# Optimization experiments

Measured on AMD Instinct MI355X. Metric: run time of the kernel, lower is better.

Reference implementation:

```python
import jax, jax.numpy as jnp
import numpy as np

E, I, H, T = 8, 2816, 1024, 8192

def setup_inputs() -> dict:
    key = jax.random.key(0)
    ks = jax.random.split(key, 5)
    scale_w = 1.0 / np.sqrt(H)
    return {
        "hidden_states": jax.random.normal(ks[0], (T, H), jnp.float32),
        "router_logits": jax.random.normal(ks[1], (T, E), jnp.float32),
        "W1": jax.random.normal(ks[2], (E, I, H), jnp.float32) * scale_w,
        "W3": jax.random.normal(ks[3], (E, I, H), jnp.float32) * scale_w,
        "W2": jax.random.normal(ks[4], (E, H, I), jnp.float32) * (1.0 / np.sqrt(I)),
        "top_k": 2,
    }

def reference(hidden_states, router_logits, W1, W3, W2, top_k):
    # softmax router in fp32, topk, renormalize (renormalize=True, use_grouped_topk=False)
    probs = jax.nn.softmax(router_logits.astype(jnp.float32), axis=-1)  # [T,E]
    vals, idx = jax.lax.top_k(probs, top_k)                             # [T,K]
    vals = vals / jnp.sum(vals, axis=-1, keepdims=True)
    vals = vals.astype(hidden_states.dtype)
    n_tok, n_exp = probs.shape
    # dense per-token expert weight matrix [T,E]; zero for unrouted experts,
    # mathematically identical to the gather/scatter-add in the ipex op
    w = jnp.zeros((n_tok, n_exp), hidden_states.dtype).at[
        jnp.arange(n_tok)[:, None], idx].add(vals)

    def expert_step(acc, args):
        We1, We3, We2, we = args  # [I,H], [I,H], [H,I], [T]
        h = jax.nn.silu(hidden_states @ We1.T) * (hidden_states @ We3.T)  # [T,I]
        return acc + we[:, None] * (h @ We2.T), None

    out, _ = jax.lax.scan(expert_step, jnp.zeros_like(hidden_states),
                          (W1, W3, W2, w.T))
    return out
```

## Files before the change

### kernel.cpp

```cpp
#include <hip/hip_runtime.h>
#include <stdint.h>

#define NE 8
#define NI 2816
#define NH 1024
#define NT 8192
#define NPAIR (NT * 2)

typedef __bf16 bf16x8 __attribute__((ext_vector_type(8)));
typedef float f32x4 __attribute__((ext_vector_type(4)));

__device__ __forceinline__ uint16_t f2bf(float f) {
    union { float f; uint32_t u; } v;
    v.f = f;
    return (uint16_t)((v.u + 0x7FFFu + ((v.u >> 16) & 1u)) >> 16);
}

__device__ __forceinline__ float bflo(uint32_t u) {
    union { uint32_t x; float f; } v; v.x = u << 16; return v.f;
}
__device__ __forceinline__ float bfhi(uint32_t u) {
    union { uint32_t x; float f; } v; v.x = u & 0xffff0000u; return v.f;
}

__device__ __forceinline__ void gld16(const void* g, void* l) {
    __builtin_amdgcn_global_load_lds(
        (__attribute__((address_space(1))) void*)(uintptr_t)g,
        (__attribute__((address_space(3))) void*)(uint32_t)(uintptr_t)l,
        16, 0, 0);
}

__global__ __launch_bounds__(256) void k_cvt_w13(const float* __restrict__ W1,
                                                 const float* __restrict__ W3,
                                                 uint16_t* __restrict__ Wg) {
    int row = blockIdx.x * 2 + (threadIdx.x >> 7);
    int g = threadIdx.x & 127;
    const float* src = (blockIdx.y == 0) ? W1 : W3;
    int e = row / NI;
    int r = row - e * NI;
    size_t drow = (size_t)e * (2 * NI) + (size_t)((r >> 4) * 32 + (r & 15) + (blockIdx.y ? 16 : 0));
    const float4* sp = (const float4*)(src + (size_t)row * NH);
    float4 a = sp[g * 2];
    float4 b = sp[g * 2 + 1];
    uint4 o;
    o.x = (uint32_t)f2bf(a.x) | ((uint32_t)f2bf(a.y) << 16);
    o.y = (uint32_t)f2bf(a.z) | ((uint32_t)f2bf(a.w) << 16);
    o.z = (uint32_t)f2bf(b.x) | ((uint32_t)f2bf(b.y) << 16);
    o.w = (uint32_t)f2bf(b.z) | ((uint32_t)f2bf(b.w) << 16);
    ((uint4*)(Wg + drow * NH))[g] = o;
}

__global__ __launch_bounds__(256) void k_cvt_flat(const float* __restrict__ S,
                                                  uint16_t* __restrict__ D) {
    size_t i = (size_t)blockIdx.x * 256 + threadIdx.x;
    float4 a = ((const float4*)S)[i * 2];
    float4 b = ((const float4*)S)[i * 2 + 1];
    uint4 o;
    o.x = (uint32_t)f2bf(a.x) | ((uint32_t)f2bf(a.y) << 16);
    o.y = (uint32_t)f2bf(a.z) | ((uint32_t)f2bf(a.w) << 16);
    o.z = (uint32_t)f2bf(b.x) | ((uint32_t)f2bf(b.y) << 16);
    o.w = (uint32_t)f2bf(b.z) | ((uint32_t)f2bf(b.w) << 16);
    ((uint4*)D)[i] = o;
}

__global__ __launch_bounds__(256) void k_router(const float* __restrict__ logits,
                                                int* __restrict__ tok_e,
                                                float2* __restrict__ tok_w,
                                                int* __restrict__ counts) {
    int t = blockIdx.x * 256 + threadIdx.x;
    if (t >= NT) return;
    float4 a = ((const float4*)logits)[(size_t)t * 2];
    float4 b = ((const float4*)logits)[(size_t)t * 2 + 1];
    float l[8] = {a.x, a.y, a.z, a.w, b.x, b.y, b.z, b.w};
    int i0 = 0; float l0 = l[0];
#pragma unroll
    for (int e = 1; e < 8; e++) if (l[e] > l0) { l0 = l[e]; i0 = e; }
    int i1 = -1; float l1 = -3.4e38f;
#pragma unroll
    for (int e = 0; e < 8; e++) if (e != i0 && l[e] > l1) { l1 = l[e]; i1 = e; }
    float w0 = 1.f / (1.f + __expf(l1 - l0));
    float w1 = 1.f - w0;
    tok_e[t] = i0 | (i1 << 8);
    tok_w[t] = make_float2(w0, w1);
    atomicAdd(&counts[i0], 1);
    atomicAdd(&counts[i1], 1);
}

__global__ void k_scan(const int* __restrict__ counts, int* __restrict__ offsets,
                       int* __restrict__ cursor) {
    if (threadIdx.x == 0) {
        int o = 0;
        for (int e = 0; e < NE; e++) { offsets[e] = o; cursor[e] = o; o += counts[e]; }
    }
}

__global__ __launch_bounds__(128) void k_gather(const float* __restrict__ x,
                                                const int* __restrict__ tok_e,
                                                const float2* __restrict__ tok_w,
                                                int* __restrict__ cursor,
                                                uint16_t* __restrict__ Xg,
                                                int2* __restrict__ tok_slots,
                                                float* __restrict__ slot_w) {
    int t = blockIdx.x;
    __shared__ int ss[2];
    if (threadIdx.x == 0) {
        int ee = tok_e[t];
        float2 w = tok_w[t];
        int s0 = atomicAdd(&cursor[ee & 0xff], 1);
        int s1 = atomicAdd(&cursor[(ee >> 8) & 0xff], 1);
        ss[0] = s0; ss[1] = s1;
        tok_slots[t] = make_int2(s0, s1);
        slot_w[s0] = w.x;
        slot_w[s1] = w.y;
    }
    __syncthreads();
    int s0 = ss[0], s1 = ss[1];
    int i = threadIdx.x;
    const float4* xr = (const float4*)(x + (size_t)t * NH);
    float4 a = xr[i * 2];
    float4 b = xr[i * 2 + 1];
    uint4 o;
    o.x = (uint32_t)f2bf(a.x) | ((uint32_t)f2bf(a.y) << 16);
    o.y = (uint32_t)f2bf(a.z) | ((uint32_t)f2bf(a.w) << 16);
    o.z = (uint32_t)f2bf(b.x) | ((uint32_t)f2bf(b.y) << 16);
    o.w = (uint32_t)f2bf(b.z) | ((uint32_t)f2bf(b.w) << 16);
    ((uint4*)(Xg + (size_t)s0 * NH))[i] = o;
    ((uint4*)(Xg + (size_t)s1 * NH))[i] = o;
}


#define BAR()  asm volatile("s_barrier" ::: "memory")
#define WAITLGKM asm volatile("s_waitcnt lgkmcnt(0)" ::: "memory")
#define WAITV4 asm volatile("s_waitcnt vmcnt(4)" ::: "memory")
#define WAITV0 asm volatile("s_waitcnt vmcnt(0)" ::: "memory")
#define SCHB __builtin_amdgcn_sched_barrier(0)
#define PRIO1 __builtin_amdgcn_s_setprio(1)
#define PRIO0 __builtin_amdgcn_s_setprio(0)

#define STAGE(ab, bufsel, h, kt)                                                  \
    do {                                                                          \
        char* d_ = lds + (bufsel) * 65536 + (ab) * 32768 + (h) * 16384 + tid * 16; \
        gld16(((ab) ? srcB : srcA)[h][0] + (kt) * 64, d_);                         \
        gld16(((ab) ? srcB : srcA)[h][1] + (kt) * 64, d_ + 8192);                  \
    } while (0)

#define READA(bufsel, mh)                                                           \
    do {                                                                            \
        _Pragma("unroll") for (int ii = 0; ii < 4; ii++) {                          \
            const char* p_ = lds + (bufsel) * 65536 + wr * 16384 +                  \
                             (((mh) * 4 + ii) * 16 + l15) * 128;                    \
            af[ii][0] = *(const bf16x8*)(p_ + colk0);                               \
            af[ii][1] = *(const bf16x8*)(p_ + colk1);                               \
        }                                                                           \
    } while (0)

#define READB(bufsel, nh, dst)                                                      \
    do {                                                                            \
        _Pragma("unroll") for (int jj = 0; jj < 2; jj++) {                          \
            int gb_ = wc * 64 + ((nh) * 2 + jj) * 16;                               \
            const char* p_ = lds + (bufsel) * 65536 + 32768 + (gb_ >> 7) * 16384 +  \
                             ((gb_ & 127) + l15) * 128;                             \
            dst[jj][0] = *(const bf16x8*)(p_ + colk0);                              \
            dst[jj][1] = *(const bf16x8*)(p_ + colk1);                              \
        }                                                                           \
    } while (0)

#define MMQ(mh, bsrc, jb)                                                           \
    do {                                                                            \
        _Pragma("unroll") for (int ii = 0; ii < 4; ii++)                            \
            _Pragma("unroll") for (int jj = 0; jj < 2; jj++)                        \
                _Pragma("unroll") for (int ks = 0; ks < 2; ks++)                    \
                    acc[(mh) * 4 + ii][(jb) + jj] =                                 \
                        __builtin_amdgcn_mfma_f32_16x16x32_bf16(                    \
                            af[ii][ks], bsrc[jj][ks], acc[(mh) * 4 + ii][(jb) + jj],\
                            0, 0, 0);                                               \
    } while (0)

#define PHASES(i2, LAST)                                                            \
    do {                                                                            \
        int t1_ = (i2) + 1, t2_ = (i2) + 2, t3_ = (i2) + 3;                         \
                                                                            \
        READA(0, 0); READB(0, 0, b0);                                               \
        STAGE(0, 1, 0, t1_); STAGE(0, 1, 1, t1_);                                   \
        BAR(); WAITLGKM; SCHB; PRIO1; MMQ(0, b0, 0); PRIO0; SCHB; BAR();            \
                                                                            \
        READB(0, 1, b1);                                                            \
        BAR(); WAITLGKM; SCHB; PRIO1; MMQ(0, b1, 2); PRIO0; SCHB; BAR();            \
                                                                            \
        READA(0, 1);                                                                \
        if (!(LAST)) STAGE(1, 0, 0, t2_);                                           \
        BAR(); WAITLGKM; SCHB; PRIO1; MMQ(1, b1, 2); PRIO0; SCHB; BAR();            \
                                                                            \
        if (!(LAST)) STAGE(1, 0, 1, t2_);                                           \
        BAR(); PRIO1; MMQ(1, b0, 0); PRIO0; SCHB;                                   \
        if (LAST) { WAITV0; } else { WAITV4; }                                      \
        BAR();                                                                      \
                                                                            \
        READA(1, 0); READB(1, 0, b0);                                               \
        if (!(LAST)) { STAGE(0, 0, 0, t2_); STAGE(0, 0, 1, t2_); }                  \
        BAR(); WAITLGKM; SCHB; PRIO1; MMQ(0, b0, 0); PRIO0; SCHB; BAR();            \
                                                                            \
        READB(1, 1, b1);                                                            \
        BAR(); WAITLGKM; SCHB; PRIO1; MMQ(0, b1, 2); PRIO0; SCHB; BAR();            \
                                                                            \
        READA(1, 1);                                                                \
        if (!(LAST)) STAGE(1, 1, 0, t3_);                                           \
        BAR(); WAITLGKM; SCHB; PRIO1; MMQ(1, b1, 2); PRIO0; SCHB; BAR();            \
                                                                            \
        if (!(LAST)) STAGE(1, 1, 1, t3_);                                           \
        BAR(); PRIO1; MMQ(1, b0, 0); PRIO0; SCHB;                                   \
        if (LAST) { WAITV0; } else { WAITV4; }                                      \
        BAR();                                                                      \
    } while (0)

template <int MODE>
__global__ __launch_bounds__(512, 2) void k_moe_gemm(const uint16_t* __restrict__ Abase,
                                                     const uint16_t* __restrict__ Bbase,
                                                     uint16_t* __restrict__ Cbase,
                                                     const int* __restrict__ counts,
                                                     const int* __restrict__ offsets) {
    constexpr int K = (MODE == 1) ? NH : NI;
    constexpr int NKT = K / 64;
    constexpr int NITER = NKT / 2;
    constexpr int BROWS = (MODE == 1) ? 2 * NI : NH;
    constexpr int CLD = (MODE == 1) ? NI : NH;

    int e = blockIdx.z;
    int n_e = counts[e];
    int mtile = blockIdx.y;
    if (mtile * 256 >= n_e) return;
    int ntile = blockIdx.x;
    int off = offsets[e];

    __shared__ __align__(16) char lds[131072];

    int tid = threadIdx.x;
    int l15 = tid & 15;
    int q = (tid >> 4) & 3;
    int x7 = tid & 7;
    int wv = tid >> 6, wr = wv >> 2, wc = wv & 3;
    int colk0 = (q ^ x7) << 4;
    int colk1 = ((q + 4) ^ x7) << 4;

    int sr = tid >> 3;
    int ss = x7 ^ (sr & 7);
    const uint16_t* srcA[2][2];
    const uint16_t* srcB[2][2];
#pragma unroll
    for (int h = 0; h < 2; h++)
#pragma unroll
        for (int j = 0; j < 2; j++) {
            int gr = off + mtile * 256 + h * 128 + j * 64 + sr;
            gr = min(gr, NPAIR - 1);
            srcA[h][j] = Abase + (size_t)gr * K + ss * 8;
            int gn = ntile * 256 + h * 128 + j * 64 + sr;
            srcB[h][j] = Bbase + (size_t)e * BROWS * K + (size_t)gn * K + ss * 8;
        }

    bf16x8 af[4][2], b0[2][2], b1[2][2];
    f32x4 acc[8][4] = {};

    STAGE(0, 0, 0, 0); STAGE(0, 0, 1, 0);
    STAGE(1, 0, 0, 0); STAGE(1, 0, 1, 0);
    STAGE(1, 1, 0, 1); STAGE(1, 1, 1, 1);
    WAITV4;
    BAR();

#pragma unroll 1
    for (int it2 = 0; it2 < NITER - 1; it2++) { PHASES(2 * it2, 0); }
    PHASES(2 * (NITER - 1), 1);

    int sBase = off + mtile * 256;
    if constexpr (MODE == 1) {
#pragma unroll
        for (int im = 0; im < 8; im++) {
#pragma unroll
            for (int r = 0; r < 4; r++) {
                int lm = wr * 128 + im * 16 + q * 4 + r;
                if (mtile * 256 + lm < n_e) {
                    uint16_t* orow = Cbase + (size_t)(sBase + lm) * CLD +
                                     ntile * 128 + wc * 32 + l15;
#pragma unroll
                    for (int j = 0; j < 2; j++) {
                        float c1 = acc[im][2 * j][r];
                        float c3 = acc[im][2 * j + 1][r];
                        float hv = (c1 / (1.f + __expf(-c1))) * c3;
                        orow[j * 16] = f2bf(hv);
                    }
                }
            }
        }
    } else {
#pragma unroll
        for (int im = 0; im < 8; im++) {
#pragma unroll
            for (int r = 0; r < 4; r++) {
                int lm = wr * 128 + im * 16 + q * 4 + r;
                if (mtile * 256 + lm < n_e) {
                    uint16_t* orow = Cbase + (size_t)(sBase + lm) * CLD +
                                     ntile * 256 + wc * 64 + l15;
#pragma unroll
                    for (int jn = 0; jn < 4; jn++) orow[jn * 16] = f2bf(acc[im][jn][r]);
                }
            }
        }
    }
}

__global__ __launch_bounds__(256) void k_combine(const uint16_t* __restrict__ Y,
                                                 const int2* __restrict__ tok_slots,
                                                 const float* __restrict__ slot_w,
                                                 float* __restrict__ out) {
    int idx = blockIdx.x * 256 + threadIdx.x;
    int t = idx >> 7;
    int g = idx & 127;
    int2 s = tok_slots[t];
    float w0 = slot_w[s.x], w1 = slot_w[s.y];
    uint4 u0 = ((const uint4*)(Y + (size_t)s.x * NH))[g];
    uint4 u1 = ((const uint4*)(Y + (size_t)s.y * NH))[g];
    float4 o0, o1;
    o0.x = w0 * bflo(u0.x) + w1 * bflo(u1.x);
    o0.y = w0 * bfhi(u0.x) + w1 * bfhi(u1.x);
    o0.z = w0 * bflo(u0.y) + w1 * bflo(u1.y);
    o0.w = w0 * bfhi(u0.y) + w1 * bfhi(u1.y);
    o1.x = w0 * bflo(u0.z) + w1 * bflo(u1.z);
    o1.y = w0 * bfhi(u0.z) + w1 * bfhi(u1.z);
    o1.z = w0 * bflo(u0.w) + w1 * bflo(u1.w);
    o1.w = w0 * bfhi(u0.w) + w1 * bfhi(u1.w);
    float4* orow = (float4*)(out + (size_t)t * NH + g * 8);
    orow[0] = o0;
    orow[1] = o1;
}

extern "C" void kernel_launch(void* const* d_in, const int* in_sizes, int n_in,
                              void* d_out, int out_size, void* d_ws, size_t ws_size,
                              hipStream_t stream) {
    const float* x = (const float*)d_in[0];
    const float* logits = (const float*)d_in[1];
    const float* W1 = (const float*)d_in[2];
    const float* W3 = (const float*)d_in[3];
    const float* W2 = (const float*)d_in[4];
    float* out = (float*)d_out;

    char* ws = (char*)d_ws;
    size_t o = 0;
    auto nxt = [&](size_t b) -> void* {
        void* p = ws + o;
        o += (b + 255) & ~(size_t)255;
        return p;
    };
    const size_t WELEMS = (size_t)NE * NI * NH;
    uint16_t* Wg = (uint16_t*)nxt(WELEMS * 2 * 2);
    uint16_t* W2b = (uint16_t*)nxt(WELEMS * 2);
    uint16_t* Xg = (uint16_t*)nxt((size_t)NPAIR * NH * 2);
    uint16_t* Hbuf = (uint16_t*)nxt((size_t)NPAIR * NI * 2);
    float* slot_w = (float*)nxt((size_t)NPAIR * 4);
    int2* tok_slots = (int2*)nxt((size_t)NT * 8);
    int* tok_e = (int*)nxt((size_t)NT * 4);
    float2* tok_w = (float2*)nxt((size_t)NT * 8);
    int* meta = (int*)nxt(128);
    int* counts = meta;
    int* offsets = meta + 8;
    int* cursor = meta + 16;
    uint16_t* Ybuf = Xg;
    (void)ws_size; (void)in_sizes; (void)n_in;

    hipMemsetAsync(meta, 0, 128, stream);

    k_router<<<NT / 256, 256, 0, stream>>>(logits, tok_e, tok_w, counts);
    k_scan<<<1, 64, 0, stream>>>(counts, offsets, cursor);

    k_cvt_w13<<<dim3(NE * NI / 2, 2), 256, 0, stream>>>(W1, W3, Wg);
    k_cvt_flat<<<(unsigned)(WELEMS / 8 / 256), 256, 0, stream>>>(W2, W2b);

    k_gather<<<NT, 128, 0, stream>>>(x, tok_e, tok_w, cursor, Xg, tok_slots, slot_w);

    k_moe_gemm<1><<<dim3(2 * NI / 256, NT / 256, NE), 512, 0, stream>>>(
        Xg, Wg, Hbuf, counts, offsets);
    k_moe_gemm<2><<<dim3(NH / 256, NT / 256, NE), 512, 0, stream>>>(
        Hbuf, W2b, Ybuf, counts, offsets);

    k_combine<<<NT * NH / 8 / 256, 256, 0, stream>>>(Ybuf, tok_slots, slot_w, out);
}
```

Baseline: 907.2 us.

## Restructure GEMM main loop into deeper staggered LDS prefetch pipeline

Replaces the two-phase PHASES macro with a single loop that issues one quarter-tile global-to-LDS stage per MFMA sub-phase and keeps more loads in flight (vmcnt 6 instead of 4). LDS reads for both B halves are issued up front and waited on partially (lgkmcnt 4), and the number of barriers per iteration drops from two per sub-phase to one. The goal is to overlap global loads and LDS reads more closely with MFMA work and cut barrier stalls. The trailing iterations clamp k-tile indices, so they issue redundant loads instead of branching, which risks extra traffic and subtle hazards from buffer reuse.

```diff
diff --git a/kernel.cpp b/kernel.cpp
--- a/kernel.cpp
+++ b/kernel.cpp
@@ -130,8 +130,9 @@
 
 
 #define BAR()  asm volatile("s_barrier" ::: "memory")
-#define WAITLGKM asm volatile("s_waitcnt lgkmcnt(0)" ::: "memory")
-#define WAITV4 asm volatile("s_waitcnt vmcnt(4)" ::: "memory")
+#define WAITLGKM0 asm volatile("s_waitcnt lgkmcnt(0)" ::: "memory")
+#define WAITLGKM4 asm volatile("s_waitcnt lgkmcnt(4)" ::: "memory")
+#define WAITV6 asm volatile("s_waitcnt vmcnt(6)" ::: "memory")
 #define WAITV0 asm volatile("s_waitcnt vmcnt(0)" ::: "memory")
 #define SCHB __builtin_amdgcn_sched_barrier(0)
 #define PRIO1 __builtin_amdgcn_s_setprio(1)
@@ -174,43 +175,6 @@
                         __builtin_amdgcn_mfma_f32_16x16x32_bf16(                    \
                             af[ii][ks], bsrc[jj][ks], acc[(mh) * 4 + ii][(jb) + jj],\
                             0, 0, 0);                                               \
-    } while (0)
-
-#define PHASES(i2, LAST)                                                            \
-    do {                                                                            \
-        int t1_ = (i2) + 1, t2_ = (i2) + 2, t3_ = (i2) + 3;                         \
-                                                                            \
-        READA(0, 0); READB(0, 0, b0);                                               \
-        STAGE(0, 1, 0, t1_); STAGE(0, 1, 1, t1_);                                   \
-        BAR(); WAITLGKM; SCHB; PRIO1; MMQ(0, b0, 0); PRIO0; SCHB; BAR();            \
-                                                                            \
-        READB(0, 1, b1);                                                            \
-        BAR(); WAITLGKM; SCHB; PRIO1; MMQ(0, b1, 2); PRIO0; SCHB; BAR();            \
-                                                                            \
-        READA(0, 1);                                                                \
-        if (!(LAST)) STAGE(1, 0, 0, t2_);                                           \
-        BAR(); WAITLGKM; SCHB; PRIO1; MMQ(1, b1, 2); PRIO0; SCHB; BAR();            \
-                                                                            \
-        if (!(LAST)) STAGE(1, 0, 1, t2_);                                           \
-        BAR(); PRIO1; MMQ(1, b0, 0); PRIO0; SCHB;                                   \
-        if (LAST) { WAITV0; } else { WAITV4; }                                      \
-        BAR();                                                                      \
-                                                                            \
-        READA(1, 0); READB(1, 0, b0);                                               \
-        if (!(LAST)) { STAGE(0, 0, 0, t2_); STAGE(0, 0, 1, t2_); }                  \
-        BAR(); WAITLGKM; SCHB; PRIO1; MMQ(0, b0, 0); PRIO0; SCHB; BAR();            \
-                                                                            \
-        READB(1, 1, b1);                                                            \
-        BAR(); WAITLGKM; SCHB; PRIO1; MMQ(0, b1, 2); PRIO0; SCHB; BAR();            \
-                                                                            \
-        READA(1, 1);                                                                \
-        if (!(LAST)) STAGE(1, 1, 0, t3_);                                           \
-        BAR(); WAITLGKM; SCHB; PRIO1; MMQ(1, b1, 2); PRIO0; SCHB; BAR();            \
-                                                                            \
-        if (!(LAST)) STAGE(1, 1, 1, t3_);                                           \
-        BAR(); PRIO1; MMQ(1, b0, 0); PRIO0; SCHB;                                   \
-        if (LAST) { WAITV0; } else { WAITV4; }                                      \
-        BAR();                                                                      \
     } while (0)
 
 template <int MODE>
@@ -260,15 +224,58 @@
     bf16x8 af[4][2], b0[2][2], b1[2][2];
     f32x4 acc[8][4] = {};
 
-    STAGE(0, 0, 0, 0); STAGE(0, 0, 1, 0);
-    STAGE(1, 0, 0, 0); STAGE(1, 0, 1, 0);
-    STAGE(1, 1, 0, 1); STAGE(1, 1, 1, 1);
-    WAITV4;
+    STAGE(1, 0, 0, 0);
+    STAGE(1, 0, 1, 0);
+    STAGE(0, 0, 0, 0);
+    STAGE(0, 0, 1, 0);
+    STAGE(1, 1, 0, 1);
+    STAGE(1, 1, 1, 1);
+    STAGE(0, 1, 0, 1);
+    WAITV6;
     BAR();
 
 #pragma unroll 1
-    for (int it2 = 0; it2 < NITER - 1; it2++) { PHASES(2 * it2, 0); }
-    PHASES(2 * (NITER - 1), 1);
+    for (int it = 0; it < NITER; ++it) {
+        int kt1 = 2 * it + 1;
+        int kt2 = min(2 * it + 2, NKT - 1);
+        int kt3 = min(2 * it + 3, NKT - 1);
+        READA(0, 0);
+        READB(0, 0, b0);
+        READB(0, 1, b1);
+        STAGE(0, 1, 1, kt1);
+        WAITLGKM4; SCHB; PRIO1; MMQ(0, b0, 0); PRIO0; SCHB;
+        BAR();
+        STAGE(1, 0, 0, kt2);
+        WAITLGKM0; SCHB; PRIO1; MMQ(0, b1, 2); PRIO0; SCHB;
+        READA(0, 1);
+        BAR();
+        STAGE(1, 0, 1, kt2);
+        WAITLGKM0; SCHB; PRIO1; MMQ(1, b1, 2); PRIO0; SCHB;
+        BAR();
+        STAGE(0, 0, 0, kt2);
+        PRIO1; MMQ(1, b0, 0); PRIO0; SCHB;
+        WAITV6;
+        BAR();
+        READA(1, 0);
+        READB(1, 0, b0);
+        READB(1, 1, b1);
+        STAGE(0, 0, 1, kt2);
+        WAITLGKM4; SCHB; PRIO1; MMQ(0, b0, 0); PRIO0; SCHB;
+        BAR();
+        STAGE(1, 1, 0, kt3);
+        WAITLGKM0; SCHB; PRIO1; MMQ(0, b1, 2); PRIO0; SCHB;
+        READA(1, 1);
+        BAR();
+        STAGE(1, 1, 1, kt3);
+        WAITLGKM0; SCHB; PRIO1; MMQ(1, b1, 2); PRIO0; SCHB;
+        BAR();
+        STAGE(0, 1, 0, kt3);
+        PRIO1; MMQ(1, b0, 0); PRIO0; SCHB;
+        WAITV6;
+        BAR();
+    }
+
+    WAITV0;
 
     int sBase = off + mtile * 256;
     if constexpr (MODE == 1) {
```

Result: faster. 885.9 us (-2.4%).
